# Performance work log

Measured on AMD Instinct MI355X. Metric: run time of the kernel, lower is better.

Reference implementation:

```python
import jax, jax.numpy as jnp
import numpy as np

B, S, DIM = 2, 2048, 1024
N_HEADS, HEAD_DIM = 16, 64
ROPE_THETA = 10000.0


def _rope_cos_sin(seq_len, head_dim, dtype=jnp.float32):
    inv_freq = 1.0 / (ROPE_THETA ** (jnp.arange(0, head_dim, 2, dtype=jnp.float32) / head_dim))
    ang = jnp.arange(seq_len, dtype=jnp.float32)[:, None] * inv_freq[None, :]  # [S, D/2]
    return jnp.cos(ang).astype(dtype), jnp.sin(ang).astype(dtype)


def _apply_rope(t, cos, sin):
    # t: [B, S, H, D]; cos/sin: [S, D/2]
    t1 = t[..., 0::2]
    t2 = t[..., 1::2]
    c = cos[None, :, None, :]
    s = sin[None, :, None, :]
    r1 = t1 * c - t2 * s
    r2 = t1 * s + t2 * c
    # interleave back to original even/odd layout
    return jnp.stack([r1, r2], axis=-1).reshape(t.shape)


def setup_inputs() -> dict:
    key = jax.random.key(0)
    ks = jax.random.split(key, 5)
    scale = 1.0 / np.sqrt(DIM)
    return {
        "x": jax.random.normal(ks[0], (B, S, DIM), dtype=jnp.float32),
        "Wq": jax.random.normal(ks[1], (DIM, DIM), dtype=jnp.float32) * scale,
        "Wk": jax.random.normal(ks[2], (DIM, DIM), dtype=jnp.float32) * scale,
        "Wv": jax.random.normal(ks[3], (DIM, DIM), dtype=jnp.float32) * scale,
        "Wo": jax.random.normal(ks[4], (DIM, DIM), dtype=jnp.float32) * scale,
    }


def reference(x, Wq, Wk, Wv, Wo):
    b, s, _ = x.shape
    q = (x @ Wq.T).reshape(b, s, N_HEADS, HEAD_DIM)
    k = (x @ Wk.T).reshape(b, s, N_HEADS, HEAD_DIM)
    v = (x @ Wv.T).reshape(b, s, N_HEADS, HEAD_DIM)

    cos, sin = _rope_cos_sin(s, HEAD_DIM, dtype=q.dtype)
    q = _apply_rope(q, cos, sin)
    k = _apply_rope(k, cos, sin)

    # [B, H, S, S] scores with causal mask
    attn = jnp.einsum("bqhd,bkhd->bhqk", q, k) / np.sqrt(HEAD_DIM)
    causal = jnp.tril(jnp.ones((s, s), dtype=bool))
    attn = jnp.where(causal[None, None], attn, jnp.float32(-jnp.inf))
    probs = jax.nn.softmax(attn.astype(jnp.float32), axis=-1).astype(q.dtype)

    out = jnp.einsum("bhqk,bkhd->bqhd", probs, v).reshape(b, s, N_HEADS * HEAD_DIM)
    return out @ Wo.T
```

## Files before the change

kernel.cpp:

```cpp
#include <hip/hip_runtime.h>
#include <hip/hip_bf16.h>

#define S_LEN 2048
#define DIMSZ 1024
#define NH    16
#define HD    64

typedef __attribute__((ext_vector_type(8))) short short8v;
typedef __attribute__((ext_vector_type(4))) short short4v;
typedef __attribute__((ext_vector_type(4))) float f32x4;

typedef const __attribute__((address_space(1))) unsigned GU;
typedef __attribute__((address_space(3))) unsigned LU;

__device__ __forceinline__ void gl16(const ushort* g, ushort* l) {
  __builtin_amdgcn_global_load_lds((GU*)g, (LU*)l, 16, 0, 0);
}

__device__ __forceinline__ ushort f2bf(float f) {
  union { float f; unsigned u; } v; v.f = f;
  unsigned u = v.u;
  return (ushort)((u + 0x7FFFu + ((u >> 16) & 1u)) >> 16);
}

__device__ __forceinline__ uint cvtpk(float lo, float hi) {
  uint d;
  asm("v_cvt_pk_bf16_f32 %0, %1, %2" : "=v"(d) : "v"(lo), "v"(hi));
  return d;
}

__global__ __launch_bounds__(256) void cvt_k(
    const float* __restrict__ x, const float* __restrict__ wq,
    const float* __restrict__ wk, const float* __restrict__ wv,
    const float* __restrict__ wo,
    ushort* __restrict__ xb, ushort* __restrict__ wqkvb, ushort* __restrict__ wob)
{
  size_t gid = (size_t)blockIdx.x * 256 + threadIdx.x;
  size_t e0 = gid * 8;
  const float* src; ushort* dst;
  if (e0 < (4u << 20)) { src = x + e0; dst = xb + e0; }
  else if (e0 < (7u << 20)) {
    size_t o = e0 - (4u << 20);
    const float* w = (o < (1u << 20)) ? wq : ((o < (2u << 20)) ? wk : wv);
    src = w + (o & ((1u << 20) - 1)); dst = wqkvb + o;
  } else {
    size_t o = e0 - (7u << 20);
    src = wo + o; dst = wob + o;
  }
  float4 a = *(const float4*)src;
  float4 b = *(const float4*)(src + 4);
  short8v h;
  h[0] = (short)f2bf(a.x); h[1] = (short)f2bf(a.y);
  h[2] = (short)f2bf(a.z); h[3] = (short)f2bf(a.w);
  h[4] = (short)f2bf(b.x); h[5] = (short)f2bf(b.y);
  h[6] = (short)f2bf(b.z); h[7] = (short)f2bf(b.w);
  *(short8v*)dst = h;
}

__global__ __launch_bounds__(256) void rope_table_k(float2* __restrict__ tab) {
  int i = blockIdx.x * 256 + threadIdx.x;
  int f = i >> 11, s = i & (S_LEN - 1);
  float inv = powf(10000.f, -(float)f * (1.f / 32.f));
  float ang = (float)s * inv;
  tab[i] = make_float2(cosf(ang), sinf(ang));
}

#define QSTAGE(c, kt_) do {                                                     \
    int k0_ = (kt_) * 64;                                                       \
    _Pragma("unroll")                                                           \
    for (int j_ = 0; j_ < 4; ++j_) {                                            \
      int R_ = w * 32 + j_ * 8;                                                 \
      gl16(xb + (size_t)(bm + R_ + r8) * DIMSZ + k0_ + cswz, &lA[c][R_ * 64]);  \
      gl16(W  + (size_t)(bn + R_ + r8) * DIMSZ + k0_ + cswz, &lB[c][R_ * 64]);  \
    }                                                                           \
  } while (0)

__global__ __launch_bounds__(256) void gemm_qkv_k(
    const ushort* __restrict__ xb, const ushort* __restrict__ wqkvb,
    ushort* __restrict__ qb, ushort* __restrict__ kb, ushort* __restrict__ vtb,
    const float2* __restrict__ rtab)
{
  __shared__ ushort lA[2][128 * 64];
  __shared__ ushort lB[2][128 * 64];
  const int t = threadIdx.x;
  int id = blockIdx.x;
  int nid = (id & 7) * 96 + (id >> 3);
  const int which = nid >> 8;
  const int bm = ((nid >> 3) & 31) * 128, bn = (nid & 7) * 128;
  const ushort* W = wqkvb + ((size_t)which << 20);
  const int w = t >> 6, l = t & 63, lr = l & 15, lg = l >> 4;
  const int wm = (w >> 1) * 64, wn = (w & 1) * 64;
  const int r8 = l >> 3;
  const int cswz = ((l & 7) ^ r8) * 8;

  f32x4 acc[4][4] = {};

  QSTAGE(0, 0);
  __syncthreads();
  for (int kt = 0; kt < DIMSZ / 64; ++kt) {
    const int cur = kt & 1;
    if (kt + 1 < DIMSZ / 64) QSTAGE(cur ^ 1, kt + 1);
    #pragma unroll
    for (int kk = 0; kk < 2; ++kk) {
      short8v a[4], b[4];
      #pragma unroll
      for (int mt = 0; mt < 4; ++mt) {
        int row = wm + mt * 16 + lr;
        a[mt] = *(const short8v*)((const char*)lA[cur] + row * 128 + ((kk * 64 + lg * 16) ^ ((row & 7) << 4)));
      }
      #pragma unroll
      for (int nt = 0; nt < 4; ++nt) {
        int row = wn + nt * 16 + lr;
        b[nt] = *(const short8v*)((const char*)lB[cur] + row * 128 + ((kk * 64 + lg * 16) ^ ((row & 7) << 4)));
      }
      #pragma unroll
      for (int mt = 0; mt < 4; ++mt)
        #pragma unroll
        for (int nt = 0; nt < 4; ++nt)
          acc[mt][nt] = __builtin_amdgcn_mfma_f32_16x16x32_bf16(b[nt], a[mt], acc[mt][nt], 0, 0, 0);
    }
    __syncthreads();
  }

  const int bb = bm >> 11, s_base = bm & (S_LEN - 1);

  if (which == 2) {
    ushort* tb = &lA[0][0];
    #pragma unroll
    for (int mt = 0; mt < 4; ++mt)
      #pragma unroll
      for (int nt = 0; nt < 4; ++nt)
        #pragma unroll
        for (int r = 0; r < 4; ++r) {
          int row = wn + nt * 16 + lg * 4 + r;
          int col = wm + mt * 16 + lr;
          int byte = row * 256 + ((col * 2) ^ (((row >> 2) & 3) << 5));
          *(ushort*)((char*)tb + byte) = f2bf(acc[mt][nt][r]);
        }
    __syncthreads();
    int row = t >> 1, half = t & 1;
    int h = (bn + row) >> 6, d = (bn + row) & 63;
    ushort* vdst = vtb + ((size_t)(bb * NH + h) * HD + d) * S_LEN + s_base + half * 64;
    #pragma unroll
    for (int j = 0; j < 8; ++j) {
      int byte = row * 256 + ((half * 128 + j * 16) ^ (((row >> 2) & 3) << 5));
      *(short8v*)(vdst + j * 8) = *(const short8v*)((const char*)tb + byte);
    }
  } else {
    ushort* dst = (which == 0) ? qb : kb;
    const float QS = (which == 0) ? (0.125f * 1.4426950408889634f) : 1.0f;
    #pragma unroll
    for (int mt = 0; mt < 4; ++mt) {
      int s = s_base + wm + mt * 16 + lr;
      #pragma unroll
      for (int nt = 0; nt < 4; ++nt) {
        int nw = bn + wn + nt * 16 + lg * 4;
        int h = nw >> 6, d0 = nw & 63;
        uint pk[2];
        #pragma unroll
        for (int rp = 0; rp < 2; ++rp) {
          float2 cs = rtab[(d0 >> 1) * S_LEN + rp * S_LEN + s];
          float t1 = acc[mt][nt][2 * rp], t2 = acc[mt][nt][2 * rp + 1];
          float o0 = (t1 * cs.x - t2 * cs.y) * QS;
          float o1 = (t1 * cs.y + t2 * cs.x) * QS;
          pk[rp] = (uint)f2bf(o0) | ((uint)f2bf(o1) << 16);
        }
        uint2 pv; pv.x = pk[0]; pv.y = pk[1];
        *(uint2*)(dst + ((size_t)(bb * NH + h) * S_LEN + s) * HD + d0) = pv;
      }
    }
  }
}

template<bool DIAG>
__device__ __forceinline__ void attn_tile(
    const ushort* lK, const ushort* lV, ushort* lPw,
    const short8v* qf, f32x4* o, float& m2, float& lsum,
    int lr, int lg, int wrow)
{
  f32x4 sacc[4] = {};
  __builtin_amdgcn_s_setprio(1);
  #pragma unroll
  for (int kk = 0; kk < 2; ++kk)
    #pragma unroll
    for (int jt = 0; jt < 4; ++jt) {
      int row = jt * 16 + lr;
      short8v kf = *(const short8v*)((const char*)lK + row * 128 + ((kk * 64 + lg * 16) ^ ((row & 7) << 4)));
      sacc[jt] = __builtin_amdgcn_mfma_f32_16x16x32_bf16(kf, qf[kk], sacc[jt], 0, 0, 0);
    }
  __builtin_amdgcn_s_setprio(0);

  float v2[4][4];
  #pragma unroll
  for (int jt = 0; jt < 4; ++jt)
    #pragma unroll
    for (int r = 0; r < 4; ++r) {
      float sv = sacc[jt][r];
      if (DIAG && (jt * 16 + lg * 4 + r > wrow + lr)) sv = -3e38f;
      v2[jt][r] = sv;
    }
  float mj[4];
  #pragma unroll
  for (int jt = 0; jt < 4; ++jt)
    mj[jt] = fmaxf(fmaxf(v2[jt][0], v2[jt][1]), fmaxf(v2[jt][2], v2[jt][3]));
  float rmax = fmaxf(fmaxf(mj[0], mj[1]), fmaxf(mj[2], mj[3]));
  rmax = fmaxf(rmax, __shfl_xor(rmax, 16));
  rmax = fmaxf(rmax, __shfl_xor(rmax, 32));

  const bool need = __any(rmax > m2 + 8.f);
  float mn = m2;
  float so = 1.f;
  if (need) {
    mn = fmaxf(m2, rmax);
    so = exp2f(m2 - mn);
    m2 = mn;
  }
  float pe[4][4];
  float ps = 0.f;
  #pragma unroll
  for (int jt = 0; jt < 4; ++jt)
    #pragma unroll
    for (int r = 0; r < 4; ++r) {
      pe[jt][r] = exp2f(v2[jt][r] - mn);
      ps += pe[jt][r];
    }
  ps += __shfl_xor(ps, 16);
  ps += __shfl_xor(ps, 32);
  if (need) {
    lsum = lsum * so + ps;
    #pragma unroll
    for (int r = 0; r < 4; ++r) {
      float sor = __shfl(so, lg * 4 + r);
      #pragma unroll
      for (int dt = 0; dt < 4; ++dt) o[dt][r] *= sor;
    }
  } else {
    lsum += ps;
  }
  #pragma unroll
  for (int jt = 0; jt < 4; ++jt) {
    uint2 pv;
    pv.x = cvtpk(pe[jt][0], pe[jt][1]);
    pv.y = cvtpk(pe[jt][2], pe[jt][3]);
    *(uint2*)((char*)lPw + lr * 128 + ((jt * 32 + lg * 8) ^ ((lr & 7) << 4))) = pv;
  }
  __builtin_amdgcn_s_setprio(1);
  #pragma unroll
  for (int kk = 0; kk < 2; ++kk) {
    short8v pa = *(const short8v*)((const char*)lPw + lr * 128 + ((kk * 64 + lg * 16) ^ ((lr & 7) << 4)));
    #pragma unroll
    for (int dt = 0; dt < 4; ++dt) {
      int row = dt * 16 + lr;
      short8v vb = *(const short8v*)((const char*)lV + row * 128 + ((kk * 64 + lg * 16) ^ ((row & 7) << 4)));
      o[dt] = __builtin_amdgcn_mfma_f32_16x16x32_bf16(pa, vb, o[dt], 0, 0, 0);
    }
  }
  __builtin_amdgcn_s_setprio(0);
}

__device__ __forceinline__ void store_tile(
    ushort* __restrict__ ab, int bh, int qt, int w, int lr, int lg,
    const f32x4* o, float lsum)
{
  int b = bh >> 4, h = bh & 15;
  #pragma unroll
  for (int r = 0; r < 4; ++r) {
    float li = __shfl(lsum, lg * 4 + r);
    float inv = 1.f / li;
    int qg = qt * 64 + w * 16 + lg * 4 + r;
    #pragma unroll
    for (int dt = 0; dt < 4; ++dt)
      ab[((size_t)b * S_LEN + qg) * DIMSZ + h * HD + dt * 16 + lr] = f2bf(o[dt][r] * inv);
  }
}

#define STAGE(c, ktile) do {                                                  \
    int kk0_ = (ktile) * 64;                                                  \
    _Pragma("unroll")                                                         \
    for (int j_ = 0; j_ < 2; ++j_) {                                          \
      int R_ = w * 16 + j_ * 8;                                               \
      gl16(kbh + (size_t)(kk0_ + R_ + r8) * HD + cswz, &lKb[c][R_ * 64]);     \
      gl16(vbh + (size_t)(R_ + r8) * S_LEN + kk0_ + cswz, &lVb[c][R_ * 64]);  \
    }                                                                         \
  } while (0)

__global__ __launch_bounds__(256) void flash_k(
    const ushort* __restrict__ qb, const ushort* __restrict__ kb,
    const ushort* __restrict__ vtb, ushort* __restrict__ ab)
{
  __shared__ ushort lKb[2][64 * 64];
  __shared__ ushort lVb[2][64 * 64];
  __shared__ ushort lP[4][16 * 64];

  int id = blockIdx.y * 16 + blockIdx.x;
  int nid = (id & 7) * 64 + (id >> 3);
  const int pr = nid & 15, bh = nid >> 4;
  const int qtA = pr, qtB = 31 - pr;
  const int NT = qtB + 1;

  const int t = threadIdx.x, w = t >> 6, l = t & 63, lr = l & 15, lg = l >> 4;
  const int r8 = l >> 3;
  const int cswz = ((l & 7) ^ r8) * 8;
  const ushort* kbh = kb + (size_t)bh * S_LEN * HD;
  const ushort* vbh = vtb + (size_t)bh * HD * S_LEN;

  short8v qfA[2], qfB[2];
  #pragma unroll
  for (int kk = 0; kk < 2; ++kk) {
    qfA[kk] = *(const short8v*)(qb + ((size_t)bh * S_LEN + qtA * 64 + w * 16 + lr) * HD + kk * 32 + lg * 8);
    qfB[kk] = *(const short8v*)(qb + ((size_t)bh * S_LEN + qtB * 64 + w * 16 + lr) * HD + kk * 32 + lg * 8);
  }

  float mA = -3e38f, lsA = 0.f, mB = -3e38f, lsB = 0.f;
  f32x4 oA[4] = {}, oB[4] = {};

  STAGE(0, 0);
  asm volatile("s_waitcnt vmcnt(0)" ::: "memory");

  for (int kt = 0; kt < NT; ++kt) {
    const int cur = kt & 1;
    if (kt + 1 < NT) {
      STAGE(cur ^ 1, kt + 1);
      asm volatile("s_waitcnt vmcnt(4)" ::: "memory");
    } else {
      asm volatile("s_waitcnt vmcnt(0)" ::: "memory");
    }
    __builtin_amdgcn_s_barrier();
    asm volatile("" ::: "memory");
    const ushort* lK = lKb[cur];
    const ushort* lV = lVb[cur];
    if (kt == qtB) attn_tile<true >(lK, lV, lP[w], qfB, oB, mB, lsB, lr, lg, w * 16);
    else           attn_tile<false>(lK, lV, lP[w], qfB, oB, mB, lsB, lr, lg, w * 16);
    if (kt <= qtA) {
      if (kt == qtA) attn_tile<true >(lK, lV, lP[w], qfA, oA, mA, lsA, lr, lg, w * 16);
      else           attn_tile<false>(lK, lV, lP[w], qfA, oA, mA, lsA, lr, lg, w * 16);
    }
    __builtin_amdgcn_s_barrier();
    asm volatile("" ::: "memory");
  }

  store_tile(ab, bh, qtB, w, lr, lg, oB, lsB);
  store_tile(ab, bh, qtA, w, lr, lg, oA, lsA);
}

#define OSTAGE(c, kt_) do {                                                     \
    int k0_ = (kt_) * 64;                                                       \
    _Pragma("unroll")                                                           \
    for (int j_ = 0; j_ < 4; ++j_) {                                            \
      int R_ = w * 32 + j_ * 8;                                                 \
      gl16(ab  + (size_t)(bm + R_ + r8) * DIMSZ + k0_ + cswz, &lA[c][R_ * 64]); \
      gl16(wob + (size_t)(bn + R_ + r8) * DIMSZ + k0_ + cswz, &lB[c][R_ * 64]); \
    }                                                                           \
  } while (0)

__global__ __launch_bounds__(256) void gemm_out_k(
    const ushort* __restrict__ ab, const ushort* __restrict__ wob, float* __restrict__ out)
{
  __shared__ ushort lA[2][128 * 64];
  __shared__ ushort lB[2][128 * 64];
  const int t = threadIdx.x;
  int id = blockIdx.x;
  int nid = (id & 7) * 32 + (id >> 3);
  const int bm = (nid >> 3) * 128, bn = (nid & 7) * 128;
  const int w = t >> 6, l = t & 63, lr = l & 15, lg = l >> 4;
  const int wm = (w >> 1) * 64, wn = (w & 1) * 64;
  const int r8 = l >> 3;
  const int cswz = ((l & 7) ^ r8) * 8;

  f32x4 acc[4][4] = {};

  OSTAGE(0, 0);
  __syncthreads();
  for (int kt = 0; kt < DIMSZ / 64; ++kt) {
    const int cur = kt & 1;
    if (kt + 1 < DIMSZ / 64) OSTAGE(cur ^ 1, kt + 1);
    #pragma unroll
    for (int kk = 0; kk < 2; ++kk) {
      short8v a[4], b[4];
      #pragma unroll
      for (int mt = 0; mt < 4; ++mt) {
        int row = wm + mt * 16 + lr;
        a[mt] = *(const short8v*)((const char*)lA[cur] + row * 128 + ((kk * 64 + lg * 16) ^ ((row & 7) << 4)));
      }
      #pragma unroll
      for (int nt = 0; nt < 4; ++nt) {
        int row = wn + nt * 16 + lr;
        b[nt] = *(const short8v*)((const char*)lB[cur] + row * 128 + ((kk * 64 + lg * 16) ^ ((row & 7) << 4)));
      }
      #pragma unroll
      for (int mt = 0; mt < 4; ++mt)
        #pragma unroll
        for (int nt = 0; nt < 4; ++nt)
          acc[mt][nt] = __builtin_amdgcn_mfma_f32_16x16x32_bf16(b[nt], a[mt], acc[mt][nt], 0, 0, 0);
    }
    __syncthreads();
  }

  #pragma unroll
  for (int mt = 0; mt < 4; ++mt) {
    int m = bm + wm + mt * 16 + lr;
    #pragma unroll
    for (int nt = 0; nt < 4; ++nt) {
      int nb = bn + wn + nt * 16 + lg * 4;
      *(f32x4*)(out + (size_t)m * DIMSZ + nb) = acc[mt][nt];
    }
  }
}

extern "C" void kernel_launch(void* const* d_in, const int* in_sizes, int n_in,
                              void* d_out, int out_size, void* d_ws, size_t ws_size,
                              hipStream_t stream) {
  (void)in_sizes; (void)n_in; (void)out_size; (void)ws_size;
  const float* x  = (const float*)d_in[0];
  const float* Wq = (const float*)d_in[1];
  const float* Wk = (const float*)d_in[2];
  const float* Wv = (const float*)d_in[3];
  const float* Wo = (const float*)d_in[4];
  float* out = (float*)d_out;

  char* ws = (char*)d_ws;
  ushort* qb    = (ushort*)(ws);
  ushort* kb    = (ushort*)(ws + ((size_t)8  << 20));
  ushort* vtb   = (ushort*)(ws + ((size_t)16 << 20));
  ushort* xb    = (ushort*)(ws + ((size_t)24 << 20));
  ushort* ab    = xb;
  ushort* wqkvb = (ushort*)(ws + ((size_t)32 << 20));
  ushort* wob   = (ushort*)(ws + ((size_t)38 << 20));
  float2* rtab  = (float2*)(ws + ((size_t)40 << 20));

  hipLaunchKernelGGL(cvt_k, dim3(4096), dim3(256), 0, stream,
                     x, Wq, Wk, Wv, Wo, xb, wqkvb, wob);
  hipLaunchKernelGGL(rope_table_k, dim3(S_LEN * 32 / 256), dim3(256), 0, stream, rtab);
  hipLaunchKernelGGL(gemm_qkv_k, dim3(768), dim3(256), 0, stream,
                     xb, wqkvb, qb, kb, vtb, rtab);
  hipLaunchKernelGGL(flash_k, dim3(16, 32), dim3(256), 0, stream, qb, kb, vtb, ab);
  hipLaunchKernelGGL(gemm_out_k, dim3(256), dim3(256), 0, stream, ab, wob, out);
}
```

Measured before the change: 138.2 us.

## Split flash-attention KV loop across two wavegroups with split-K merge

The flash kernel now runs 512 threads as two groups of four waves. Each group processes alternating KV tiles from a flattened list of 33 work items (32-pr tiles for query tile B, pr+1 for A), halving the serial loop depth to 17 rounds. Partial outputs and running max/sum are written to LDS and merged with log-sum-exp rescaling before the bf16 store. This doubles LDS usage and adds a final merge step in exchange for more parallelism per block.

```diff
diff --git a/kernel.cpp b/kernel.cpp
--- a/kernel.cpp
+++ b/kernel.cpp
@@ -258,89 +258,117 @@
   __builtin_amdgcn_s_setprio(0);
 }
 
-__device__ __forceinline__ void store_tile(
-    ushort* __restrict__ ab, int bh, int qt, int w, int lr, int lg,
-    const f32x4* o, float lsum)
-{
-  int b = bh >> 4, h = bh & 15;
-  #pragma unroll
-  for (int r = 0; r < 4; ++r) {
-    float li = __shfl(lsum, lg * 4 + r);
-    float inv = 1.f / li;
-    int qg = qt * 64 + w * 16 + lg * 4 + r;
-    #pragma unroll
-    for (int dt = 0; dt < 4; ++dt)
-      ab[((size_t)b * S_LEN + qg) * DIMSZ + h * HD + dt * 16 + lr] = f2bf(o[dt][r] * inv);
-  }
-}
-
-#define STAGE(c, ktile) do {                                                  \
-    int kk0_ = (ktile) * 64;                                                  \
-    _Pragma("unroll")                                                         \
-    for (int j_ = 0; j_ < 2; ++j_) {                                          \
-      int R_ = w * 16 + j_ * 8;                                               \
-      gl16(kbh + (size_t)(kk0_ + R_ + r8) * HD + cswz, &lKb[c][R_ * 64]);     \
-      gl16(vbh + (size_t)(R_ + r8) * S_LEN + kk0_ + cswz, &lVb[c][R_ * 64]);  \
-    }                                                                         \
+#define ITEM_KT(i_) (((i_) <= qtB) ? (i_) : ((i_) - qtB - 1))
+
+#define FSTAGE(c, rnd) do {                                                   \
+    int i0_ = (rnd) * 2, i1_ = i0_ + 1;                                       \
+    int ka_ = ITEM_KT(i0_) * 64;                                              \
+    int kb_ = ((i1_ <= 32) ? ITEM_KT(i1_) : 0) * 64;                          \
+    gl16(kbh + (size_t)(ka_ + trow) * HD + cswz,    &lKb[c][0][w * 512]);     \
+    gl16(kbh + (size_t)(kb_ + trow) * HD + cswz,    &lKb[c][1][w * 512]);     \
+    gl16(vbh + (size_t)trow * S_LEN + ka_ + cswz,   &lVb[c][0][w * 512]);     \
+    gl16(vbh + (size_t)trow * S_LEN + kb_ + cswz,   &lVb[c][1][w * 512]);     \
   } while (0)
 
-__global__ __launch_bounds__(256) void flash_k(
+__global__ __launch_bounds__(512, 4) void flash_k(
     const ushort* __restrict__ qb, const ushort* __restrict__ kb,
     const ushort* __restrict__ vtb, ushort* __restrict__ ab)
 {
-  __shared__ ushort lKb[2][64 * 64];
-  __shared__ ushort lVb[2][64 * 64];
-  __shared__ ushort lP[4][16 * 64];
+  __shared__ ushort lKb[2][2][64 * 64];
+  __shared__ ushort lVb[2][2][64 * 64];
+  __shared__ ushort lP[8][16 * 64];
 
   int id = blockIdx.y * 16 + blockIdx.x;
   int nid = (id & 7) * 64 + (id >> 3);
   const int pr = nid & 15, bh = nid >> 4;
   const int qtA = pr, qtB = 31 - pr;
-  const int NT = qtB + 1;
 
   const int t = threadIdx.x, w = t >> 6, l = t & 63, lr = l & 15, lg = l >> 4;
+  const int g = w >> 2, ws = w & 3;
   const int r8 = l >> 3;
   const int cswz = ((l & 7) ^ r8) * 8;
+  const int trow = t >> 3;
   const ushort* kbh = kb + (size_t)bh * S_LEN * HD;
   const ushort* vbh = vtb + (size_t)bh * HD * S_LEN;
 
   short8v qfA[2], qfB[2];
   #pragma unroll
   for (int kk = 0; kk < 2; ++kk) {
-    qfA[kk] = *(const short8v*)(qb + ((size_t)bh * S_LEN + qtA * 64 + w * 16 + lr) * HD + kk * 32 + lg * 8);
-    qfB[kk] = *(const short8v*)(qb + ((size_t)bh * S_LEN + qtB * 64 + w * 16 + lr) * HD + kk * 32 + lg * 8);
+    qfA[kk] = *(const short8v*)(qb + ((size_t)bh * S_LEN + qtA * 64 + ws * 16 + lr) * HD + kk * 32 + lg * 8);
+    qfB[kk] = *(const short8v*)(qb + ((size_t)bh * S_LEN + qtB * 64 + ws * 16 + lr) * HD + kk * 32 + lg * 8);
   }
 
   float mA = -3e38f, lsA = 0.f, mB = -3e38f, lsB = 0.f;
   f32x4 oA[4] = {}, oB[4] = {};
 
-  STAGE(0, 0);
+  FSTAGE(0, 0);
   asm volatile("s_waitcnt vmcnt(0)" ::: "memory");
 
-  for (int kt = 0; kt < NT; ++kt) {
-    const int cur = kt & 1;
-    if (kt + 1 < NT) {
-      STAGE(cur ^ 1, kt + 1);
+  const int NR = 17;
+  for (int rnd = 0; rnd < NR; ++rnd) {
+    const int cur = rnd & 1;
+    if (rnd + 1 < NR) {
+      FSTAGE(cur ^ 1, rnd + 1);
       asm volatile("s_waitcnt vmcnt(4)" ::: "memory");
     } else {
       asm volatile("s_waitcnt vmcnt(0)" ::: "memory");
     }
     __builtin_amdgcn_s_barrier();
     asm volatile("" ::: "memory");
-    const ushort* lK = lKb[cur];
-    const ushort* lV = lVb[cur];
-    if (kt == qtB) attn_tile<true >(lK, lV, lP[w], qfB, oB, mB, lsB, lr, lg, w * 16);
-    else           attn_tile<false>(lK, lV, lP[w], qfB, oB, mB, lsB, lr, lg, w * 16);
-    if (kt <= qtA) {
-      if (kt == qtA) attn_tile<true >(lK, lV, lP[w], qfA, oA, mA, lsA, lr, lg, w * 16);
-      else           attn_tile<false>(lK, lV, lP[w], qfA, oA, mA, lsA, lr, lg, w * 16);
+    const int it = 2 * rnd + g;
+    if (it <= 32) {
+      const ushort* lK = lKb[cur][g];
+      const ushort* lV = lVb[cur][g];
+      if (it <= qtB) {
+        if (it == qtB) attn_tile<true >(lK, lV, lP[w], qfB, oB, mB, lsB, lr, lg, ws * 16);
+        else           attn_tile<false>(lK, lV, lP[w], qfB, oB, mB, lsB, lr, lg, ws * 16);
+      } else {
+        const int ka = it - qtB - 1;
+        if (ka == qtA) attn_tile<true >(lK, lV, lP[w], qfA, oA, mA, lsA, lr, lg, ws * 16);
+        else           attn_tile<false>(lK, lV, lP[w], qfA, oA, mA, lsA, lr, lg, ws * 16);
+      }
     }
     __builtin_amdgcn_s_barrier();
     asm volatile("" ::: "memory");
   }
 
-  store_tile(ab, bh, qtB, w, lr, lg, oB, lsB);
-  store_tile(ab, bh, qtA, w, lr, lg, oA, lsA);
+  float* obB = (float*)&lKb[0][0][0];
+  float* obA = (float*)&lVb[0][0][0];
+  float* ml  = (float*)&lP[0][0];
+  const int blk = g * 4 + ws;
+  #pragma unroll
+  for (int dt = 0; dt < 4; ++dt)
+    #pragma unroll
+    for (int r = 0; r < 4; ++r) {
+      obB[blk * 1024 + (lg * 4 + r) * 64 + dt * 16 + lr] = oB[dt][r];
+      obA[blk * 1024 + (lg * 4 + r) * 64 + dt * 16 + lr] = oA[dt][r];
+    }
+  if (lg == 0) {
+    ml[(blk * 16 + lr) * 2 + 0] = mB;  ml[(blk * 16 + lr) * 2 + 1] = lsB;
+    ml[512 + (blk * 16 + lr) * 2 + 0] = mA;  ml[512 + (blk * 16 + lr) * 2 + 1] = lsA;
+  }
+  __syncthreads();
+
+  const float* mlm = ml + (g ? 512 : 0);
+  const float* o0  = (g ? obA : obB) + ws * 1024;
+  const float* o1  = (g ? obA : obB) + (4 + ws) * 1024;
+  const int qt = g ? qtA : qtB;
+  const int b = bh >> 4, h = bh & 15;
+  #pragma unroll
+  for (int r = 0; r < 4; ++r) {
+    int row = lg * 4 + r;
+    float m0 = mlm[(ws * 16 + row) * 2 + 0], l0 = mlm[(ws * 16 + row) * 2 + 1];
+    float m1 = mlm[((4 + ws) * 16 + row) * 2 + 0], l1 = mlm[((4 + ws) * 16 + row) * 2 + 1];
+    float msr = fmaxf(m0, m1);
+    float a0 = exp2f(m0 - msr), a1 = exp2f(m1 - msr);
+    float inv = 1.f / (l0 * a0 + l1 * a1);
+    int qg = qt * 64 + ws * 16 + row;
+    #pragma unroll
+    for (int dt = 0; dt < 4; ++dt) {
+      float v = o0[row * 64 + dt * 16 + lr] * a0 + o1[row * 64 + dt * 16 + lr] * a1;
+      ab[((size_t)b * S_LEN + qg) * DIMSZ + h * HD + dt * 16 + lr] = f2bf(v * inv);
+    }
+  }
 }
 
 #define OSTAGE(c, kt_) do {                                                     \
@@ -433,6 +461,6 @@
   hipLaunchKernelGGL(rope_table_k, dim3(S_LEN * 32 / 256), dim3(256), 0, stream, rtab);
   hipLaunchKernelGGL(gemm_qkv_k, dim3(768), dim3(256), 0, stream,
                      xb, wqkvb, qb, kb, vtb, rtab);
-  hipLaunchKernelGGL(flash_k, dim3(16, 32), dim3(256), 0, stream, qb, kb, vtb, ab);
+  hipLaunchKernelGGL(flash_k, dim3(16, 32), dim3(512), 0, stream, qb, kb, vtb, ab);
   hipLaunchKernelGGL(gemm_out_k, dim3(256), dim3(256), 0, stream, ab, wob, out);
 }
```

Measured after the change: 132.0 us. 4.5% less time.

## Split paired causal q-tiles into one tile per block, longest-first order

Applied to the files above, without the earlier changes.

The flash attention kernel used to give each block a balanced pair of query tiles (qt and 31-qt) that share K/V staging. Now each block handles a single query tile, the grid doubles to 1024 blocks, and blocks are ordered so the longest causal tiles launch first. A minimum of 4 blocks per CU is requested through launch bounds. The aim is more parallelism, lower per-block register use and better occupancy, at the cost of K/V tiles no longer being reused across two query tiles and unequal block lengths that depend on the scheduler to balance.

```diff
diff --git a/kernel.cpp b/kernel.cpp
--- a/kernel.cpp
+++ b/kernel.cpp
@@ -284,7 +284,7 @@
     }                                                                         \
   } while (0)
 
-__global__ __launch_bounds__(256) void flash_k(
+__global__ __launch_bounds__(256, 4) void flash_k(
     const ushort* __restrict__ qb, const ushort* __restrict__ kb,
     const ushort* __restrict__ vtb, ushort* __restrict__ ab)
 {
@@ -292,11 +292,11 @@
   __shared__ ushort lVb[2][64 * 64];
   __shared__ ushort lP[4][16 * 64];
 
-  int id = blockIdx.y * 16 + blockIdx.x;
-  int nid = (id & 7) * 64 + (id >> 3);
-  const int pr = nid & 15, bh = nid >> 4;
-  const int qtA = pr, qtB = 31 - pr;
-  const int NT = qtB + 1;
+  int id = blockIdx.x;
+  int nid = (id & 7) * 128 + (id >> 3);
+  const int bh = (nid >> 7) * 4 + (nid & 3);
+  const int qt = 31 - ((nid & 127) >> 2);
+  const int NT = qt + 1;
 
   const int t = threadIdx.x, w = t >> 6, l = t & 63, lr = l & 15, lg = l >> 4;
   const int r8 = l >> 3;
@@ -304,15 +304,13 @@
   const ushort* kbh = kb + (size_t)bh * S_LEN * HD;
   const ushort* vbh = vtb + (size_t)bh * HD * S_LEN;
 
-  short8v qfA[2], qfB[2];
-  #pragma unroll
-  for (int kk = 0; kk < 2; ++kk) {
-    qfA[kk] = *(const short8v*)(qb + ((size_t)bh * S_LEN + qtA * 64 + w * 16 + lr) * HD + kk * 32 + lg * 8);
-    qfB[kk] = *(const short8v*)(qb + ((size_t)bh * S_LEN + qtB * 64 + w * 16 + lr) * HD + kk * 32 + lg * 8);
-  }
-
-  float mA = -3e38f, lsA = 0.f, mB = -3e38f, lsB = 0.f;
-  f32x4 oA[4] = {}, oB[4] = {};
+  short8v qf[2];
+  #pragma unroll
+  for (int kk = 0; kk < 2; ++kk)
+    qf[kk] = *(const short8v*)(qb + ((size_t)bh * S_LEN + qt * 64 + w * 16 + lr) * HD + kk * 32 + lg * 8);
+
+  float m2 = -3e38f, lsum = 0.f;
+  f32x4 o[4] = {};
 
   STAGE(0, 0);
   asm volatile("s_waitcnt vmcnt(0)" ::: "memory");
@@ -329,18 +327,13 @@
     asm volatile("" ::: "memory");
     const ushort* lK = lKb[cur];
     const ushort* lV = lVb[cur];
-    if (kt == qtB) attn_tile<true >(lK, lV, lP[w], qfB, oB, mB, lsB, lr, lg, w * 16);
-    else           attn_tile<false>(lK, lV, lP[w], qfB, oB, mB, lsB, lr, lg, w * 16);
-    if (kt <= qtA) {
-      if (kt == qtA) attn_tile<true >(lK, lV, lP[w], qfA, oA, mA, lsA, lr, lg, w * 16);
-      else           attn_tile<false>(lK, lV, lP[w], qfA, oA, mA, lsA, lr, lg, w * 16);
-    }
+    if (kt == qt) attn_tile<true >(lK, lV, lP[w], qf, o, m2, lsum, lr, lg, w * 16);
+    else          attn_tile<false>(lK, lV, lP[w], qf, o, m2, lsum, lr, lg, w * 16);
     __builtin_amdgcn_s_barrier();
     asm volatile("" ::: "memory");
   }
 
-  store_tile(ab, bh, qtB, w, lr, lg, oB, lsB);
-  store_tile(ab, bh, qtA, w, lr, lg, oA, lsA);
+  store_tile(ab, bh, qt, w, lr, lg, o, lsum);
 }
 
 #define OSTAGE(c, kt_) do {                                                     \
@@ -433,6 +426,6 @@
   hipLaunchKernelGGL(rope_table_k, dim3(S_LEN * 32 / 256), dim3(256), 0, stream, rtab);
   hipLaunchKernelGGL(gemm_qkv_k, dim3(768), dim3(256), 0, stream,
                      xb, wqkvb, qb, kb, vtb, rtab);
-  hipLaunchKernelGGL(flash_k, dim3(16, 32), dim3(256), 0, stream, qb, kb, vtb, ab);
+  hipLaunchKernelGGL(flash_k, dim3(1024), dim3(256), 0, stream, qb, kb, vtb, ab);
   hipLaunchKernelGGL(gemm_out_k, dim3(256), dim3(256), 0, stream, ab, wob, out);
 }
```

Result: faster. 132.7 us (-4.0%).
